# Optimization experiments

Hardware: AMD Instinct MI355X
Metric: run time of the kernel (lower is better)

The kernel has to match this reference:

```python
import jax, jax.numpy as jnp
import numpy as np

N, D, H = 4096, 1024, 16
GAMMA = 1.0


def setup_inputs() -> dict:
    key = jax.random.key(0)
    ks = jax.random.split(key, 10)
    s = 1.0 / np.sqrt(D)
    return {
        "x": jax.random.normal(ks[0], (N, D), jnp.float32),
        "h": jax.random.normal(ks[1], (N,), jnp.float32),
        "Wq": jax.random.normal(ks[2], (D, D), jnp.float32) * s,
        "bq": jax.random.normal(ks[3], (D,), jnp.float32) * s,
        "Wk": jax.random.normal(ks[4], (D, D), jnp.float32) * s,
        "bk": jax.random.normal(ks[5], (D,), jnp.float32) * s,
        "Wv": jax.random.normal(ks[6], (D, D), jnp.float32) * s,
        "bv": jax.random.normal(ks[7], (D,), jnp.float32) * s,
        "Wo": jax.random.normal(ks[8], (D, D), jnp.float32) * s,
        "bo": jax.random.normal(ks[9], (D,), jnp.float32) * s,
    }


def reference(x, h, Wq, bq, Wk, bk, Wv, bv, Wo, bo):
    n, d = x.shape
    d_head = d // H
    # torch Linear: y = x @ W.T + b
    q = (x @ Wq.T + bq).reshape(n, H, d_head)
    k = (x @ Wk.T + bk).reshape(n, H, d_head)
    v = (x @ Wv.T + bv).reshape(n, H, d_head)
    scale = 1.0 / np.sqrt(d_head).astype(np.float32)
    logits = jnp.einsum('nhd,mhd->hnm', q, k) * scale  # (H, n, n)
    logits = logits - (GAMMA * h)[None, None, :]       # per-key additive bias
    attn = jax.nn.softmax(logits, axis=-1)
    out = jnp.einsum('hnm,mhd->nhd', attn, v).reshape(n, d)
    return out @ Wo.T + bo + x
```

## Files before the change

### kernel.cpp

```cpp
#include <hip/hip_runtime.h>
#include <hip/hip_bf16.h>
#include <stdint.h>

#define NTOK 4096
#define DM   1024
#define NH   16
#define DH   64
#define SCL  0.1803368801111129f
#define LOG2E 1.4426950408889634f

typedef __attribute__((ext_vector_type(8)))  short bf16x8;
typedef __attribute__((ext_vector_type(4)))  float f32x4;
typedef __attribute__((ext_vector_type(16))) float f32x16;
typedef __attribute__((ext_vector_type(4)))  unsigned short us4;

__device__ inline unsigned short f2bf(float f) {
  union { float f; unsigned int u; } a;
  a.f = f;
  unsigned int u = a.u;
  u += 0x7fffu + ((u >> 16) & 1u);
  return (unsigned short)(u >> 16);
}

__device__ inline unsigned int cvtpk_bf16(float lo, float hi) {
  unsigned int r;
  asm("v_cvt_pk_bf16_f32 %0, %1, %2" : "=v"(r) : "v"(lo), "v"(hi));
  return r;
}

__device__ inline void gload_lds16(const void* gsrc, void* ldst) {
  __builtin_amdgcn_global_load_lds(
      (const __attribute__((address_space(1))) void*)(uintptr_t)gsrc,
      (__attribute__((address_space(3))) void*)(unsigned int)(uintptr_t)ldst,
      16, 0, 0);
}

__global__ void cvt_kernel(const float* __restrict__ in,
                           unsigned short* __restrict__ out, int n4) {
  int i = blockIdx.x * 256 + threadIdx.x;
  if (i < n4) {
    float4 v = ((const float4*)in)[i];
    us4 o;
    o[0] = f2bf(v.x); o[1] = f2bf(v.y); o[2] = f2bf(v.z); o[3] = f2bf(v.w);
    ((us4*)out)[i] = o;
  }
}

__global__ void hprep_kernel(const float* __restrict__ h,
                             float* __restrict__ hperm) {
  int i = blockIdx.x * 256 + threadIdx.x;
  int r  = i & 15;
  int hi = (i >> 4) & 1;
  int t  = i >> 5;
  int key = t * 32 + (r & 3) + 8 * (r >> 2) + 4 * hi;
  hperm[i] = -LOG2E * h[key];
}

__global__ __launch_bounds__(256)
void gemm_qkv(const unsigned short* __restrict__ A,
              const unsigned short* __restrict__ B,
              const float* __restrict__ bq, const float* __restrict__ bk,
              const float* __restrict__ bv,
              unsigned short* __restrict__ Qb, unsigned short* __restrict__ Kb,
              unsigned short* __restrict__ Vt)
{
  const int tid  = threadIdx.x;
  const int wid  = tid >> 6;
  const int lane = tid & 63;
  const int bn = blockIdx.x * 128;
  const int bm = blockIdx.y * 128;
  const int wr = wid >> 1;
  const int wc = wid & 1;

  __shared__ __align__(16) unsigned short As[128 * 32];
  __shared__ __align__(16) unsigned short Bs[128 * 32];

  f32x4 acc[4][4];
#pragma unroll
  for (int i = 0; i < 4; i++)
#pragma unroll
    for (int j = 0; j < 4; j++) acc[i][j] = f32x4{0.f, 0.f, 0.f, 0.f};

  const int fr = lane & 15;
  const int fk = (lane >> 4) * 8;
  const int srow = lane >> 2;
  const int scol = (lane & 3) * 8;

  for (int k0 = 0; k0 < DM; k0 += 32) {
#pragma unroll
    for (int c = 0; c < 2; ++c) {
      const int chunk = wid * 2 + c;
      gload_lds16(A + (size_t)(bm + chunk * 16 + srow) * DM + k0 + scol,
                  &As[chunk * 512]);
      gload_lds16(B + (size_t)(bn + chunk * 16 + srow) * DM + k0 + scol,
                  &Bs[chunk * 512]);
    }
    __syncthreads();
    bf16x8 af[4], bfr[4];
#pragma unroll
    for (int i = 0; i < 4; i++)
      af[i] = *(const bf16x8*)&As[(wr * 64 + i * 16 + fr) * 32 + fk];
#pragma unroll
    for (int j = 0; j < 4; j++)
      bfr[j] = *(const bf16x8*)&Bs[(wc * 64 + j * 16 + fr) * 32 + fk];
#pragma unroll
    for (int i = 0; i < 4; i++)
#pragma unroll
      for (int j = 0; j < 4; j++)
        acc[i][j] = __builtin_amdgcn_mfma_f32_16x16x32_bf16(af[i], bfr[j],
                                                            acc[i][j], 0, 0, 0);
    __syncthreads();
  }

  const int fq = lane >> 4;
  const int region = bn >> 10;
  const float* bias = (region == 0) ? bq : (region == 1) ? bk : bv;
  const float qscale = (region == 0) ? SCL : 1.0f;
  unsigned short* outp = (region == 0) ? Qb : Kb;
#pragma unroll
  for (int j = 0; j < 4; j++) {
    const int col = bn + wc * 64 + j * 16 + fr;
    const int cl  = col & 1023;
    const float bvx = bias[cl];
#pragma unroll
    for (int i = 0; i < 4; i++) {
      const int row0 = bm + wr * 64 + i * 16 + fq * 4;
      if (region < 2) {
#pragma unroll
        for (int r = 0; r < 4; r++)
          outp[(size_t)(row0 + r) * DM + cl] = f2bf((acc[i][j][r] + bvx) * qscale);
      } else {
        us4 pk;
#pragma unroll
        for (int r = 0; r < 4; r++) pk[r] = f2bf(acc[i][j][r] + bvx);
        *(us4*)&Vt[(size_t)cl * NTOK + row0] = pk;
      }
    }
  }
}

__global__ __launch_bounds__(256)
void gemm_out(const unsigned short* __restrict__ A,
              const unsigned short* __restrict__ B,
              const float* __restrict__ bias,
              const float* __restrict__ resid,
              float* __restrict__ Cf)
{
  const int tid  = threadIdx.x;
  const int wid  = tid >> 6;
  const int lane = tid & 63;
  const int bn = blockIdx.x * 128;
  const int bm = blockIdx.y * 128;
  const int wr = wid >> 1;
  const int wc = wid & 1;

  __shared__ __align__(16) unsigned short As[128 * 32];
  __shared__ __align__(16) unsigned short Bs[128 * 32];

  f32x4 acc[4][4];
#pragma unroll
  for (int i = 0; i < 4; i++)
#pragma unroll
    for (int j = 0; j < 4; j++) acc[i][j] = f32x4{0.f, 0.f, 0.f, 0.f};

  const int fr = lane & 15;
  const int fk = (lane >> 4) * 8;
  const int srow = lane >> 2;
  const int scol = (lane & 3) * 8;

  for (int k0 = 0; k0 < DM; k0 += 32) {
#pragma unroll
    for (int c = 0; c < 2; ++c) {
      const int chunk = wid * 2 + c;
      gload_lds16(A + (size_t)(bm + chunk * 16 + srow) * DM + k0 + scol,
                  &As[chunk * 512]);
      gload_lds16(B + (size_t)(bn + chunk * 16 + srow) * DM + k0 + scol,
                  &Bs[chunk * 512]);
    }
    __syncthreads();
    bf16x8 af[4], bfr[4];
#pragma unroll
    for (int i = 0; i < 4; i++)
      af[i] = *(const bf16x8*)&As[(wr * 64 + i * 16 + fr) * 32 + fk];
#pragma unroll
    for (int j = 0; j < 4; j++)
      bfr[j] = *(const bf16x8*)&Bs[(wc * 64 + j * 16 + fr) * 32 + fk];
#pragma unroll
    for (int i = 0; i < 4; i++)
#pragma unroll
      for (int j = 0; j < 4; j++)
        acc[i][j] = __builtin_amdgcn_mfma_f32_16x16x32_bf16(af[i], bfr[j],
                                                            acc[i][j], 0, 0, 0);
    __syncthreads();
  }

  const int fq = lane >> 4;
#pragma unroll
  for (int j = 0; j < 4; j++) {
    const int col = bn + wc * 64 + j * 16 + fr;
    const float bvx = bias[col];
#pragma unroll
    for (int i = 0; i < 4; i++) {
      const int row0 = bm + wr * 64 + i * 16 + fq * 4;
#pragma unroll
      for (int r = 0; r < 4; r++) {
        const size_t idx = (size_t)(row0 + r) * DM + col;
        Cf[idx] = acc[i][j][r] + bvx + resid[idx];
      }
    }
  }
}

#define MFMA32(a, b, c) __builtin_amdgcn_mfma_f32_32x32x16_bf16(a, b, c, 0, 0, 0)

__global__ void attn_kernel(const unsigned short* __restrict__ Q,
                            const unsigned short* __restrict__ K,
                            const unsigned short* __restrict__ Vt,
                            const float* __restrict__ hperm,
                            unsigned short* __restrict__ O)
{
  const int wgid = (blockIdx.x & 7) * 64 + (blockIdx.x >> 3);
  const int head = wgid >> 5;
  const int tid  = threadIdx.x;
  const int wid  = tid >> 6;
  const int grp  = wid >> 2;
  const int w4   = wid & 3;
  const int lane = tid & 63;
  const int c31  = lane & 31;
  const int hi   = lane >> 5;
  const int qb   = (wgid & 31) * 128 + w4 * 32;
  const int k0g  = grp * (NTOK / 4);

  __shared__ __align__(16) char lds_raw[65536];
  char* kbase = lds_raw + grp * 16384;
  char* vbase = kbase + 8192;

  const int l8 = lane >> 3;
  const int l7 = lane & 7;
  const int sq = l7 ^ l8;
  const unsigned short* kg =
      K + (size_t)(k0g + w4 * 8 + l8) * DM + head * DH + sq * 8;
  const unsigned short* vg =
      Vt + (size_t)(head * DH + (sq >> 2) * 32 + w4 * 8 + l8) * NTOK
         + k0g + (sq & 3) * 8;

  int koffB[4], voffB[2][2];
#pragma unroll
  for (int f = 0; f < 4; f++)
    koffB[f] = c31 * 128 + (((f * 2 + hi) ^ (c31 & 7)) << 4);
#pragma unroll
  for (int db = 0; db < 2; db++)
#pragma unroll
    for (int ko = 0; ko < 2; ko++)
      voffB[db][ko] = c31 * 128 + (((db * 4 + ko * 2 + hi) ^ (c31 & 7)) << 4);

  const unsigned short* qp = Q + (size_t)(qb + c31) * DM + head * DH + hi * 8;
  const bf16x8 qf0 = *(const bf16x8*)(qp);
  const bf16x8 qf1 = *(const bf16x8*)(qp + 16);
  const bf16x8 qf2 = *(const bf16x8*)(qp + 32);
  const bf16x8 qf3 = *(const bf16x8*)(qp + 48);

  f32x16 o0, o1;
#pragma unroll
  for (int i = 0; i < 16; i++) { o0[i] = 0.f; o1[i] = 0.f; }
  float l = 0.f;

  gload_lds16(kg, kbase + w4 * 1024);
  gload_lds16(vg, vbase + w4 * 1024);
  __syncthreads();

  int cur = 0;
  const int NT = NTOK / 4 / 32;
  for (int t = 0; t < NT; ++t) {
    if (t + 1 < NT) {
      gload_lds16(kg + (size_t)(t + 1) * 32 * DM,
                  kbase + (cur ^ 1) * 4096 + w4 * 1024);
      gload_lds16(vg + (t + 1) * 32,
                  vbase + (cur ^ 1) * 4096 + w4 * 1024);
    }

    const float* hp = hperm + k0g + t * 32 + hi * 16;
    const float4 b0 = *(const float4*)(hp + 0);
    const float4 b1 = *(const float4*)(hp + 4);
    const float4 b2 = *(const float4*)(hp + 8);
    const float4 b3 = *(const float4*)(hp + 12);
    f32x16 s;
    s[0]  = b0.x; s[1]  = b0.y; s[2]  = b0.z; s[3]  = b0.w;
    s[4]  = b1.x; s[5]  = b1.y; s[6]  = b1.z; s[7]  = b1.w;
    s[8]  = b2.x; s[9]  = b2.y; s[10] = b2.z; s[11] = b2.w;
    s[12] = b3.x; s[13] = b3.y; s[14] = b3.z; s[15] = b3.w;

    const char* Kb = kbase + cur * 4096;
    const char* Vb = vbase + cur * 4096;
    const bf16x8 kf0 = *(const bf16x8*)(Kb + koffB[0]);
    const bf16x8 kf1 = *(const bf16x8*)(Kb + koffB[1]);
    const bf16x8 kf2 = *(const bf16x8*)(Kb + koffB[2]);
    const bf16x8 kf3 = *(const bf16x8*)(Kb + koffB[3]);
    const bf16x8 v00 = *(const bf16x8*)(Vb + voffB[0][0]);
    const bf16x8 v01 = *(const bf16x8*)(Vb + voffB[0][1]);
    const bf16x8 v10 = *(const bf16x8*)(Vb + voffB[1][0]);
    const bf16x8 v11 = *(const bf16x8*)(Vb + voffB[1][1]);

    s = MFMA32(kf0, qf0, s);
    s = MFMA32(kf1, qf1, s);
    s = MFMA32(kf2, qf2, s);
    s = MFMA32(kf3, qf3, s);

    float ps[16];
#pragma unroll
    for (int r = 0; r < 16; r++) ps[r] = __builtin_amdgcn_exp2f(s[r]);
    const float rs = (((ps[0] + ps[1]) + (ps[2] + ps[3])) +
                      ((ps[4] + ps[5]) + (ps[6] + ps[7]))) +
                     (((ps[8] + ps[9]) + (ps[10] + ps[11])) +
                      ((ps[12] + ps[13]) + (ps[14] + ps[15])));
    l += rs;

    unsigned int X1 = cvtpk_bf16(ps[0],  ps[1]);
    unsigned int X2 = cvtpk_bf16(ps[2],  ps[3]);
    unsigned int Y1 = cvtpk_bf16(ps[4],  ps[5]);
    unsigned int Y2 = cvtpk_bf16(ps[6],  ps[7]);
    asm("v_permlane32_swap_b32 %0, %1" : "+v"(X1), "+v"(Y1));
    asm("v_permlane32_swap_b32 %0, %1" : "+v"(X2), "+v"(Y2));
    unsigned int X3 = cvtpk_bf16(ps[8],  ps[9]);
    unsigned int X4 = cvtpk_bf16(ps[10], ps[11]);
    unsigned int Y3 = cvtpk_bf16(ps[12], ps[13]);
    unsigned int Y4 = cvtpk_bf16(ps[14], ps[15]);
    asm("v_permlane32_swap_b32 %0, %1" : "+v"(X3), "+v"(Y3));
    asm("v_permlane32_swap_b32 %0, %1" : "+v"(X4), "+v"(Y4));

    union { unsigned int u[4]; bf16x8 v; } P0, P1;
    P0.u[0] = X1; P0.u[1] = X2; P0.u[2] = Y1; P0.u[3] = Y2;
    P1.u[0] = X3; P1.u[1] = X4; P1.u[2] = Y3; P1.u[3] = Y4;

    o0 = MFMA32(v00, P0.v, o0);
    o0 = MFMA32(v01, P1.v, o0);
    o1 = MFMA32(v10, P0.v, o1);
    o1 = MFMA32(v11, P1.v, o1);

    __syncthreads();
    cur ^= 1;
  }

  float ov[32];
#pragma unroll
  for (int i = 0; i < 16; i++) { ov[i] = o0[i]; ov[16 + i] = o1[i]; }
  l += __shfl_xor(l, 32, 64);

  float* mO = (float*)lds_raw;
  float* mL = (float*)(lds_raw + 34816);
  const int g2 = grp >> 1;
  float* slotA = &mO[((g2 * 4 + w4) * 64 + lane) * 17];
  const int liA = (g2 * 4 + w4) * 32 + c31;
  float* slotB = &mO[(w4 * 64 + lane) * 17];
  const int liB = w4 * 32 + c31;

#pragma unroll
  for (int H = 0; H < 2; H++) {
    if (grp & 1) {
#pragma unroll
      for (int i = 0; i < 16; i++) slotA[i] = ov[H * 16 + i];
      if (H == 0 && hi == 0) mL[liA] = l;
    }
    __syncthreads();
    if (!(grp & 1)) {
#pragma unroll
      for (int i = 0; i < 16; i++) ov[H * 16 + i] += slotA[i];
      if (H == 0) l += mL[liA];
    }
    __syncthreads();
  }
#pragma unroll
  for (int H = 0; H < 2; H++) {
    if (grp == 2) {
#pragma unroll
      for (int i = 0; i < 16; i++) slotB[i] = ov[H * 16 + i];
      if (H == 0 && hi == 0) mL[liB] = l;
    }
    __syncthreads();
    if (grp == 0) {
#pragma unroll
      for (int i = 0; i < 16; i++) ov[H * 16 + i] += slotB[i];
      if (H == 0) l += mL[liB];
    }
    __syncthreads();
  }

  if (grp == 0) {
    const float inv = 1.0f / l;
    unsigned short* ob = O + (size_t)(qb + c31) * DM + head * DH;
#pragma unroll
    for (int g = 0; g < 4; g++) {
      us4 pk;
      pk[0] = f2bf(ov[4 * g + 0] * inv); pk[1] = f2bf(ov[4 * g + 1] * inv);
      pk[2] = f2bf(ov[4 * g + 2] * inv); pk[3] = f2bf(ov[4 * g + 3] * inv);
      *(us4*)(ob + 8 * g + 4 * hi) = pk;
    }
#pragma unroll
    for (int g = 0; g < 4; g++) {
      us4 pk;
      pk[0] = f2bf(ov[16 + 4 * g + 0] * inv); pk[1] = f2bf(ov[16 + 4 * g + 1] * inv);
      pk[2] = f2bf(ov[16 + 4 * g + 2] * inv); pk[3] = f2bf(ov[16 + 4 * g + 3] * inv);
      *(us4*)(ob + 32 + 8 * g + 4 * hi) = pk;
    }
  }
}

extern "C" void kernel_launch(void* const* d_in, const int* in_sizes, int n_in,
                              void* d_out, int out_size, void* d_ws, size_t ws_size,
                              hipStream_t stream) {
  const float* x  = (const float*)d_in[0];
  const float* h  = (const float*)d_in[1];
  const float* Wq = (const float*)d_in[2];
  const float* bq = (const float*)d_in[3];
  const float* Wk = (const float*)d_in[4];
  const float* bk = (const float*)d_in[5];
  const float* Wv = (const float*)d_in[6];
  const float* bv = (const float*)d_in[7];
  const float* Wo = (const float*)d_in[8];
  const float* bo = (const float*)d_in[9];
  float* out = (float*)d_out;

  char* ws = (char*)d_ws;
  const size_t MB = 1 << 20;
  unsigned short* xb    = (unsigned short*)(ws + 0 * MB);
  unsigned short* wqkvb = (unsigned short*)(ws + 8 * MB);
  unsigned short* wob   = (unsigned short*)(ws + 14 * MB);
  unsigned short* Qb    = (unsigned short*)(ws + 16 * MB);
  unsigned short* Kb    = (unsigned short*)(ws + 24 * MB);
  unsigned short* Vtb   = (unsigned short*)(ws + 32 * MB);
  unsigned short* AOb   = (unsigned short*)(ws + 40 * MB);
  float*          hperm = (float*)(ws + 48 * MB);

  cvt_kernel<<<4096, 256, 0, stream>>>(x,  xb, (NTOK * DM) / 4);
  cvt_kernel<<<1024, 256, 0, stream>>>(Wq, wqkvb,               (DM * DM) / 4);
  cvt_kernel<<<1024, 256, 0, stream>>>(Wk, wqkvb + DM * DM,     (DM * DM) / 4);
  cvt_kernel<<<1024, 256, 0, stream>>>(Wv, wqkvb + 2 * DM * DM, (DM * DM) / 4);
  cvt_kernel<<<1024, 256, 0, stream>>>(Wo, wob,                 (DM * DM) / 4);
  hprep_kernel<<<16, 256, 0, stream>>>(h, hperm);

  gemm_qkv<<<dim3(24, 32), 256, 0, stream>>>(xb, wqkvb, bq, bk, bv, Qb, Kb, Vtb);

  attn_kernel<<<dim3(512), 1024, 0, stream>>>(Qb, Kb, Vtb, hperm, AOb);

  gemm_out<<<dim3(DM / 128, NTOK / 128), 256, 0, stream>>>(AOb, wob, bo, x, out);
}
```

Measured before the change: 188.0 us.

## Double query rows per wave in attention and fuse conversion kernels

The attention kernel now has each wave process two 32-row query tiles, A and B, against every K/V tile loaded into LDS. The block shrinks to 512 threads with two key-split groups, and the grid goes from 512 blocks to 256. Halving the redundant K/V loads and LDS reads per unit of MFMA work should improve reuse and shorten the cross-group reduction, at the cost of more registers and fewer blocks in flight. Separately, the five dtype conversion launches and the h-permutation launch are merged into one fused kernel to cut launch overhead.

```diff
diff --git a/kernel.cpp b/kernel.cpp
--- a/kernel.cpp
+++ b/kernel.cpp
@@ -35,25 +35,37 @@
       16, 0, 0);
 }
 
-__global__ void cvt_kernel(const float* __restrict__ in,
-                           unsigned short* __restrict__ out, int n4) {
-  int i = blockIdx.x * 256 + threadIdx.x;
-  if (i < n4) {
-    float4 v = ((const float4*)in)[i];
-    us4 o;
-    o[0] = f2bf(v.x); o[1] = f2bf(v.y); o[2] = f2bf(v.z); o[3] = f2bf(v.w);
-    ((us4*)out)[i] = o;
-  }
-}
-
-__global__ void hprep_kernel(const float* __restrict__ h,
-                             float* __restrict__ hperm) {
-  int i = blockIdx.x * 256 + threadIdx.x;
-  int r  = i & 15;
-  int hi = (i >> 4) & 1;
-  int t  = i >> 5;
-  int key = t * 32 + (r & 3) + 8 * (r >> 2) + 4 * hi;
-  hperm[i] = -LOG2E * h[key];
+__global__ void cvt_fused(const float* __restrict__ x,
+                          const float* __restrict__ Wq,
+                          const float* __restrict__ Wk,
+                          const float* __restrict__ Wv,
+                          const float* __restrict__ Wo,
+                          const float* __restrict__ h,
+                          unsigned short* __restrict__ xb,
+                          unsigned short* __restrict__ wqkvb,
+                          unsigned short* __restrict__ wob,
+                          float* __restrict__ hperm) {
+  const int b = blockIdx.x;
+  if (b >= 8192) {
+    int i = (b - 8192) * 256 + threadIdx.x;
+    int r  = i & 15;
+    int hh = (i >> 4) & 1;
+    int t  = i >> 5;
+    int key = t * 32 + (r & 3) + 8 * (r >> 2) + 4 * hh;
+    hperm[i] = -LOG2E * h[key];
+    return;
+  }
+  int i = b * 256 + threadIdx.x;
+  const float* src; unsigned short* dst; int off;
+  if (i < 1048576)      { src = x;  dst = xb;                 off = i; }
+  else if (i < 1310720) { src = Wq; dst = wqkvb;              off = i - 1048576; }
+  else if (i < 1572864) { src = Wk; dst = wqkvb + DM * DM;    off = i - 1310720; }
+  else if (i < 1835008) { src = Wv; dst = wqkvb + 2 * DM * DM; off = i - 1572864; }
+  else                  { src = Wo; dst = wob;                off = i - 1835008; }
+  float4 v = ((const float4*)src)[off];
+  us4 o;
+  o[0] = f2bf(v.x); o[1] = f2bf(v.y); o[2] = f2bf(v.z); o[3] = f2bf(v.w);
+  ((us4*)dst)[off] = o;
 }
 
 __global__ __launch_bounds__(256)
@@ -213,14 +225,16 @@
 
 #define MFMA32(a, b, c) __builtin_amdgcn_mfma_f32_32x32x16_bf16(a, b, c, 0, 0, 0)
 
-__global__ void attn_kernel(const unsigned short* __restrict__ Q,
-                            const unsigned short* __restrict__ K,
-                            const unsigned short* __restrict__ Vt,
-                            const float* __restrict__ hperm,
-                            unsigned short* __restrict__ O)
+__global__ __launch_bounds__(512)
+void attn_kernel(const unsigned short* __restrict__ Q,
+                 const unsigned short* __restrict__ K,
+                 const unsigned short* __restrict__ Vt,
+                 const float* __restrict__ hperm,
+                 unsigned short* __restrict__ O)
 {
-  const int wgid = (blockIdx.x & 7) * 64 + (blockIdx.x >> 3);
-  const int head = wgid >> 5;
+  const int wgid = (blockIdx.x & 7) * 32 + (blockIdx.x >> 3);
+  const int head = wgid >> 4;
+  const int qblk = wgid & 15;
   const int tid  = threadIdx.x;
   const int wid  = tid >> 6;
   const int grp  = wid >> 2;
@@ -228,49 +242,58 @@
   const int lane = tid & 63;
   const int c31  = lane & 31;
   const int hi   = lane >> 5;
-  const int qb   = (wgid & 31) * 128 + w4 * 32;
-  const int k0g  = grp * (NTOK / 4);
-
-  __shared__ __align__(16) char lds_raw[65536];
+  const int qwb  = qblk * 256 + w4 * 64;
+  const int k0g  = grp * 2048;
+
+  __shared__ __align__(16) char lds_raw[34816];
   char* kbase = lds_raw + grp * 16384;
   char* vbase = kbase + 8192;
 
-  const int l8 = lane >> 3;
-  const int l7 = lane & 7;
-  const int sq = l7 ^ l8;
+  const int srow = w4 * 4 + (lane >> 4);
+  const int ssl  = lane & 15;
+  const int kq   = ssl ^ srow;
+  const int kkey = srow + 16 * (kq >> 3);
   const unsigned short* kg =
-      K + (size_t)(k0g + w4 * 8 + l8) * DM + head * DH + sq * 8;
+      K + (size_t)(k0g + kkey) * DM + head * DH + (kq & 7) * 8;
+  const int vd = ((kq) >> 2) * 16 + srow;
   const unsigned short* vg =
-      Vt + (size_t)(head * DH + (sq >> 2) * 32 + w4 * 8 + l8) * NTOK
-         + k0g + (sq & 3) * 8;
-
+      Vt + (size_t)(head * DH + vd) * NTOK + k0g + (kq & 3) * 8;
+
+  const int fr15 = c31 & 15;
+  const int fkh  = c31 >> 4;
   int koffB[4], voffB[2][2];
 #pragma unroll
   for (int f = 0; f < 4; f++)
-    koffB[f] = c31 * 128 + (((f * 2 + hi) ^ (c31 & 7)) << 4);
+    koffB[f] = fr15 * 256 + (((fkh * 8 + f * 2 + hi) ^ fr15) << 4);
 #pragma unroll
   for (int db = 0; db < 2; db++)
 #pragma unroll
     for (int ko = 0; ko < 2; ko++)
-      voffB[db][ko] = c31 * 128 + (((db * 4 + ko * 2 + hi) ^ (c31 & 7)) << 4);
-
-  const unsigned short* qp = Q + (size_t)(qb + c31) * DM + head * DH + hi * 8;
-  const bf16x8 qf0 = *(const bf16x8*)(qp);
-  const bf16x8 qf1 = *(const bf16x8*)(qp + 16);
-  const bf16x8 qf2 = *(const bf16x8*)(qp + 32);
-  const bf16x8 qf3 = *(const bf16x8*)(qp + 48);
-
-  f32x16 o0, o1;
-#pragma unroll
-  for (int i = 0; i < 16; i++) { o0[i] = 0.f; o1[i] = 0.f; }
-  float l = 0.f;
+      voffB[db][ko] =
+          fr15 * 256 + ((((db * 2 + fkh) * 4 + ko * 2 + hi) ^ fr15) << 4);
+
+  const unsigned short* qpA = Q + (size_t)(qwb + c31) * DM + head * DH + hi * 8;
+  const unsigned short* qpB = qpA + (size_t)32 * DM;
+  const bf16x8 qa0 = *(const bf16x8*)(qpA);
+  const bf16x8 qa1 = *(const bf16x8*)(qpA + 16);
+  const bf16x8 qa2 = *(const bf16x8*)(qpA + 32);
+  const bf16x8 qa3 = *(const bf16x8*)(qpA + 48);
+  const bf16x8 qb0 = *(const bf16x8*)(qpB);
+  const bf16x8 qb1 = *(const bf16x8*)(qpB + 16);
+  const bf16x8 qb2 = *(const bf16x8*)(qpB + 32);
+  const bf16x8 qb3 = *(const bf16x8*)(qpB + 48);
+
+  f32x16 o0A, o1A, o0B, o1B;
+#pragma unroll
+  for (int i = 0; i < 16; i++) { o0A[i] = 0.f; o1A[i] = 0.f; o0B[i] = 0.f; o1B[i] = 0.f; }
+  float lA = 0.f, lB = 0.f;
 
   gload_lds16(kg, kbase + w4 * 1024);
   gload_lds16(vg, vbase + w4 * 1024);
   __syncthreads();
 
   int cur = 0;
-  const int NT = NTOK / 4 / 32;
+  const int NT = 2048 / 32;
   for (int t = 0; t < NT; ++t) {
     if (t + 1 < NT) {
       gload_lds16(kg + (size_t)(t + 1) * 32 * DM,
@@ -284,11 +307,6 @@
     const float4 b1 = *(const float4*)(hp + 4);
     const float4 b2 = *(const float4*)(hp + 8);
     const float4 b3 = *(const float4*)(hp + 12);
-    f32x16 s;
-    s[0]  = b0.x; s[1]  = b0.y; s[2]  = b0.z; s[3]  = b0.w;
-    s[4]  = b1.x; s[5]  = b1.y; s[6]  = b1.z; s[7]  = b1.w;
-    s[8]  = b2.x; s[9]  = b2.y; s[10] = b2.z; s[11] = b2.w;
-    s[12] = b3.x; s[13] = b3.y; s[14] = b3.z; s[15] = b3.w;
 
     const char* Kb = kbase + cur * 4096;
     const char* Vb = vbase + cur * 4096;
@@ -296,25 +314,35 @@
     const bf16x8 kf1 = *(const bf16x8*)(Kb + koffB[1]);
     const bf16x8 kf2 = *(const bf16x8*)(Kb + koffB[2]);
     const bf16x8 kf3 = *(const bf16x8*)(Kb + koffB[3]);
+
+    f32x16 sA, sB;
+    sA[0]  = b0.x; sA[1]  = b0.y; sA[2]  = b0.z; sA[3]  = b0.w;
+    sA[4]  = b1.x; sA[5]  = b1.y; sA[6]  = b1.z; sA[7]  = b1.w;
+    sA[8]  = b2.x; sA[9]  = b2.y; sA[10] = b2.z; sA[11] = b2.w;
+    sA[12] = b3.x; sA[13] = b3.y; sA[14] = b3.z; sA[15] = b3.w;
+    sB = sA;
+
+    sA = MFMA32(kf0, qa0, sA);
+    sA = MFMA32(kf1, qa1, sA);
+    sA = MFMA32(kf2, qa2, sA);
+    sA = MFMA32(kf3, qa3, sA);
+    sB = MFMA32(kf0, qb0, sB);
+    sB = MFMA32(kf1, qb1, sB);
+    sB = MFMA32(kf2, qb2, sB);
+    sB = MFMA32(kf3, qb3, sB);
+
     const bf16x8 v00 = *(const bf16x8*)(Vb + voffB[0][0]);
     const bf16x8 v01 = *(const bf16x8*)(Vb + voffB[0][1]);
     const bf16x8 v10 = *(const bf16x8*)(Vb + voffB[1][0]);
     const bf16x8 v11 = *(const bf16x8*)(Vb + voffB[1][1]);
 
-    s = MFMA32(kf0, qf0, s);
-    s = MFMA32(kf1, qf1, s);
-    s = MFMA32(kf2, qf2, s);
-    s = MFMA32(kf3, qf3, s);
-
     float ps[16];
 #pragma unroll
-    for (int r = 0; r < 16; r++) ps[r] = __builtin_amdgcn_exp2f(s[r]);
-    const float rs = (((ps[0] + ps[1]) + (ps[2] + ps[3])) +
-                      ((ps[4] + ps[5]) + (ps[6] + ps[7]))) +
-                     (((ps[8] + ps[9]) + (ps[10] + ps[11])) +
-                      ((ps[12] + ps[13]) + (ps[14] + ps[15])));
-    l += rs;
-
+    for (int r = 0; r < 16; r++) ps[r] = __builtin_amdgcn_exp2f(sA[r]);
+    lA += (((ps[0] + ps[1]) + (ps[2] + ps[3])) +
+           ((ps[4] + ps[5]) + (ps[6] + ps[7]))) +
+          (((ps[8] + ps[9]) + (ps[10] + ps[11])) +
+           ((ps[12] + ps[13]) + (ps[14] + ps[15])));
     unsigned int X1 = cvtpk_bf16(ps[0],  ps[1]);
     unsigned int X2 = cvtpk_bf16(ps[2],  ps[3]);
     unsigned int Y1 = cvtpk_bf16(ps[4],  ps[5]);
@@ -327,80 +355,97 @@
     unsigned int Y4 = cvtpk_bf16(ps[14], ps[15]);
     asm("v_permlane32_swap_b32 %0, %1" : "+v"(X3), "+v"(Y3));
     asm("v_permlane32_swap_b32 %0, %1" : "+v"(X4), "+v"(Y4));
-
-    union { unsigned int u[4]; bf16x8 v; } P0, P1;
-    P0.u[0] = X1; P0.u[1] = X2; P0.u[2] = Y1; P0.u[3] = Y2;
-    P1.u[0] = X3; P1.u[1] = X4; P1.u[2] = Y3; P1.u[3] = Y4;
-
-    o0 = MFMA32(v00, P0.v, o0);
-    o0 = MFMA32(v01, P1.v, o0);
-    o1 = MFMA32(v10, P0.v, o1);
-    o1 = MFMA32(v11, P1.v, o1);
+    union { unsigned int u[4]; bf16x8 v; } PA0, PA1;
+    PA0.u[0] = X1; PA0.u[1] = X2; PA0.u[2] = Y1; PA0.u[3] = Y2;
+    PA1.u[0] = X3; PA1.u[1] = X4; PA1.u[2] = Y3; PA1.u[3] = Y4;
+
+#pragma unroll
+    for (int r = 0; r < 16; r++) ps[r] = __builtin_amdgcn_exp2f(sB[r]);
+    lB += (((ps[0] + ps[1]) + (ps[2] + ps[3])) +
+           ((ps[4] + ps[5]) + (ps[6] + ps[7]))) +
+          (((ps[8] + ps[9]) + (ps[10] + ps[11])) +
+           ((ps[12] + ps[13]) + (ps[14] + ps[15])));
+    X1 = cvtpk_bf16(ps[0],  ps[1]);
+    X2 = cvtpk_bf16(ps[2],  ps[3]);
+    Y1 = cvtpk_bf16(ps[4],  ps[5]);
+    Y2 = cvtpk_bf16(ps[6],  ps[7]);
+    asm("v_permlane32_swap_b32 %0, %1" : "+v"(X1), "+v"(Y1));
+    asm("v_permlane32_swap_b32 %0, %1" : "+v"(X2), "+v"(Y2));
+    X3 = cvtpk_bf16(ps[8],  ps[9]);
+    X4 = cvtpk_bf16(ps[10], ps[11]);
+    Y3 = cvtpk_bf16(ps[12], ps[13]);
+    Y4 = cvtpk_bf16(ps[14], ps[15]);
+    asm("v_permlane32_swap_b32 %0, %1" : "+v"(X3), "+v"(Y3));
+    asm("v_permlane32_swap_b32 %0, %1" : "+v"(X4), "+v"(Y4));
+    union { unsigned int u[4]; bf16x8 v; } PB0, PB1;
+    PB0.u[0] = X1; PB0.u[1] = X2; PB0.u[2] = Y1; PB0.u[3] = Y2;
+    PB1.u[0] = X3; PB1.u[1] = X4; PB1.u[2] = Y3; PB1.u[3] = Y4;
+
+    o0A = MFMA32(v00, PA0.v, o0A);
+    o0A = MFMA32(v01, PA1.v, o0A);
+    o1A = MFMA32(v10, PA0.v, o1A);
+    o1A = MFMA32(v11, PA1.v, o1A);
+    o0B = MFMA32(v00, PB0.v, o0B);
+    o0B = MFMA32(v01, PB1.v, o0B);
+    o1B = MFMA32(v10, PB0.v, o1B);
+    o1B = MFMA32(v11, PB1.v, o1B);
 
     __syncthreads();
     cur ^= 1;
   }
 
-  float ov[32];
-#pragma unroll
-  for (int i = 0; i < 16; i++) { ov[i] = o0[i]; ov[16 + i] = o1[i]; }
-  l += __shfl_xor(l, 32, 64);
-
-  float* mO = (float*)lds_raw;
-  float* mL = (float*)(lds_raw + 34816);
-  const int g2 = grp >> 1;
-  float* slotA = &mO[((g2 * 4 + w4) * 64 + lane) * 17];
-  const int liA = (g2 * 4 + w4) * 32 + c31;
-  float* slotB = &mO[(w4 * 64 + lane) * 17];
-  const int liB = w4 * 32 + c31;
-
-#pragma unroll
-  for (int H = 0; H < 2; H++) {
-    if (grp & 1) {
-#pragma unroll
-      for (int i = 0; i < 16; i++) slotA[i] = ov[H * 16 + i];
-      if (H == 0 && hi == 0) mL[liA] = l;
-    }
-    __syncthreads();
-    if (!(grp & 1)) {
-#pragma unroll
-      for (int i = 0; i < 16; i++) ov[H * 16 + i] += slotA[i];
-      if (H == 0) l += mL[liA];
-    }
-    __syncthreads();
-  }
-#pragma unroll
-  for (int H = 0; H < 2; H++) {
-    if (grp == 2) {
-#pragma unroll
-      for (int i = 0; i < 16; i++) slotB[i] = ov[H * 16 + i];
-      if (H == 0 && hi == 0) mL[liB] = l;
+  lA += __shfl_xor(lA, 32, 64);
+  lB += __shfl_xor(lB, 32, 64);
+
+  float* mo = (float*)lds_raw;
+  float* mL = (float*)(lds_raw + 33792);
+  float* row = &mo[(w4 * 64 + lane) * 33];
+#pragma unroll
+  for (int half = 0; half < 2; half++) {
+    __syncthreads();
+    if (grp == 1) {
+      const f32x16& hA = half ? o1A : o0A;
+      const f32x16& hB = half ? o1B : o0B;
+#pragma unroll
+      for (int i = 0; i < 16; i++) { row[i] = hA[i]; row[16 + i] = hB[i]; }
+      if (half == 0 && hi == 0) {
+        mL[(w4 * 2 + 0) * 32 + c31] = lA;
+        mL[(w4 * 2 + 1) * 32 + c31] = lB;
+      }
     }
     __syncthreads();
     if (grp == 0) {
-#pragma unroll
-      for (int i = 0; i < 16; i++) ov[H * 16 + i] += slotB[i];
-      if (H == 0) l += mL[liB];
-    }
-    __syncthreads();
+      f32x16& hA = half ? o1A : o0A;
+      f32x16& hB = half ? o1B : o0B;
+#pragma unroll
+      for (int i = 0; i < 16; i++) { hA[i] += row[i]; hB[i] += row[16 + i]; }
+      if (half == 0) {
+        lA += mL[(w4 * 2 + 0) * 32 + c31];
+        lB += mL[(w4 * 2 + 1) * 32 + c31];
+      }
+    }
   }
 
   if (grp == 0) {
-    const float inv = 1.0f / l;
-    unsigned short* ob = O + (size_t)(qb + c31) * DM + head * DH;
+    const float invA = 1.0f / lA;
+    const float invB = 1.0f / lB;
+    unsigned short* obA = O + (size_t)(qwb + c31) * DM + head * DH;
+    unsigned short* obB = obA + (size_t)32 * DM;
 #pragma unroll
     for (int g = 0; g < 4; g++) {
       us4 pk;
-      pk[0] = f2bf(ov[4 * g + 0] * inv); pk[1] = f2bf(ov[4 * g + 1] * inv);
-      pk[2] = f2bf(ov[4 * g + 2] * inv); pk[3] = f2bf(ov[4 * g + 3] * inv);
-      *(us4*)(ob + 8 * g + 4 * hi) = pk;
-    }
-#pragma unroll
-    for (int g = 0; g < 4; g++) {
-      us4 pk;
-      pk[0] = f2bf(ov[16 + 4 * g + 0] * inv); pk[1] = f2bf(ov[16 + 4 * g + 1] * inv);
-      pk[2] = f2bf(ov[16 + 4 * g + 2] * inv); pk[3] = f2bf(ov[16 + 4 * g + 3] * inv);
-      *(us4*)(ob + 32 + 8 * g + 4 * hi) = pk;
+      pk[0] = f2bf(o0A[4 * g + 0] * invA); pk[1] = f2bf(o0A[4 * g + 1] * invA);
+      pk[2] = f2bf(o0A[4 * g + 2] * invA); pk[3] = f2bf(o0A[4 * g + 3] * invA);
+      *(us4*)(obA + 8 * g + 4 * hi) = pk;
+      pk[0] = f2bf(o1A[4 * g + 0] * invA); pk[1] = f2bf(o1A[4 * g + 1] * invA);
+      pk[2] = f2bf(o1A[4 * g + 2] * invA); pk[3] = f2bf(o1A[4 * g + 3] * invA);
+      *(us4*)(obA + 32 + 8 * g + 4 * hi) = pk;
+      pk[0] = f2bf(o0B[4 * g + 0] * invB); pk[1] = f2bf(o0B[4 * g + 1] * invB);
+      pk[2] = f2bf(o0B[4 * g + 2] * invB); pk[3] = f2bf(o0B[4 * g + 3] * invB);
+      *(us4*)(obB + 8 * g + 4 * hi) = pk;
+      pk[0] = f2bf(o1B[4 * g + 0] * invB); pk[1] = f2bf(o1B[4 * g + 1] * invB);
+      pk[2] = f2bf(o1B[4 * g + 2] * invB); pk[3] = f2bf(o1B[4 * g + 3] * invB);
+      *(us4*)(obB + 32 + 8 * g + 4 * hi) = pk;
     }
   }
 }
@@ -431,16 +476,12 @@
   unsigned short* AOb   = (unsigned short*)(ws + 40 * MB);
   float*          hperm = (float*)(ws + 48 * MB);
 
-  cvt_kernel<<<4096, 256, 0, stream>>>(x,  xb, (NTOK * DM) / 4);
-  cvt_kernel<<<1024, 256, 0, stream>>>(Wq, wqkvb,               (DM * DM) / 4);
-  cvt_kernel<<<1024, 256, 0, stream>>>(Wk, wqkvb + DM * DM,     (DM * DM) / 4);
-  cvt_kernel<<<1024, 256, 0, stream>>>(Wv, wqkvb + 2 * DM * DM, (DM * DM) / 4);
-  cvt_kernel<<<1024, 256, 0, stream>>>(Wo, wob,                 (DM * DM) / 4);
-  hprep_kernel<<<16, 256, 0, stream>>>(h, hperm);
+  cvt_fused<<<8208, 256, 0, stream>>>(x, Wq, Wk, Wv, Wo, h,
+                                      xb, wqkvb, wob, hperm);
 
   gemm_qkv<<<dim3(24, 32), 256, 0, stream>>>(xb, wqkvb, bq, bk, bv, Qb, Kb, Vtb);
 
-  attn_kernel<<<dim3(512), 1024, 0, stream>>>(Qb, Kb, Vtb, hperm, AOb);
+  attn_kernel<<<dim3(256), 512, 0, stream>>>(Qb, Kb, Vtb, hperm, AOb);
 
   gemm_out<<<dim3(DM / 128, NTOK / 128), 256, 0, stream>>>(AOb, wob, bo, x, out);
 }
```

Measured after the change: 169.2 us. 1.11x faster.

## Halve attention workgroup to two key groups and fuse conversion kernels

Applied to the files above, without the earlier changes.

The attention kernel drops from 1024 to 512 threads per workgroup, so two key-split groups of 2048 keys each run instead of four groups of 1024. LDS shrinks to 32KB, the K/V staging layout and swizzle change to a 16-row pattern, and the cross-group reduction becomes a single step. The five fp32-to-bf16 conversion launches and the h-prep launch are merged into one kernel to cut launch overhead. Each workgroup now runs longer serial loops with fewer waves, but smaller LDS and launch bounds could allow more workgroups per CU.

```diff
diff --git a/kernel.cpp b/kernel.cpp
--- a/kernel.cpp
+++ b/kernel.cpp
@@ -35,25 +35,37 @@
       16, 0, 0);
 }
 
-__global__ void cvt_kernel(const float* __restrict__ in,
-                           unsigned short* __restrict__ out, int n4) {
-  int i = blockIdx.x * 256 + threadIdx.x;
-  if (i < n4) {
-    float4 v = ((const float4*)in)[i];
-    us4 o;
-    o[0] = f2bf(v.x); o[1] = f2bf(v.y); o[2] = f2bf(v.z); o[3] = f2bf(v.w);
-    ((us4*)out)[i] = o;
-  }
-}
-
-__global__ void hprep_kernel(const float* __restrict__ h,
-                             float* __restrict__ hperm) {
-  int i = blockIdx.x * 256 + threadIdx.x;
-  int r  = i & 15;
-  int hi = (i >> 4) & 1;
-  int t  = i >> 5;
-  int key = t * 32 + (r & 3) + 8 * (r >> 2) + 4 * hi;
-  hperm[i] = -LOG2E * h[key];
+__global__ void cvt_fused(const float* __restrict__ x,
+                          const float* __restrict__ Wq,
+                          const float* __restrict__ Wk,
+                          const float* __restrict__ Wv,
+                          const float* __restrict__ Wo,
+                          const float* __restrict__ h,
+                          unsigned short* __restrict__ xb,
+                          unsigned short* __restrict__ wqkvb,
+                          unsigned short* __restrict__ wob,
+                          float* __restrict__ hperm) {
+  const int b = blockIdx.x;
+  if (b >= 8192) {
+    int i = (b - 8192) * 256 + threadIdx.x;
+    int r  = i & 15;
+    int hh = (i >> 4) & 1;
+    int t  = i >> 5;
+    int key = t * 32 + (r & 3) + 8 * (r >> 2) + 4 * hh;
+    hperm[i] = -LOG2E * h[key];
+    return;
+  }
+  int i = b * 256 + threadIdx.x;
+  const float* src; unsigned short* dst; int off;
+  if (i < 1048576)      { src = x;  dst = xb;                 off = i; }
+  else if (i < 1310720) { src = Wq; dst = wqkvb;              off = i - 1048576; }
+  else if (i < 1572864) { src = Wk; dst = wqkvb + DM * DM;    off = i - 1310720; }
+  else if (i < 1835008) { src = Wv; dst = wqkvb + 2 * DM * DM; off = i - 1572864; }
+  else                  { src = Wo; dst = wob;                off = i - 1835008; }
+  float4 v = ((const float4*)src)[off];
+  us4 o;
+  o[0] = f2bf(v.x); o[1] = f2bf(v.y); o[2] = f2bf(v.z); o[3] = f2bf(v.w);
+  ((us4*)dst)[off] = o;
 }
 
 __global__ __launch_bounds__(256)
@@ -213,14 +225,16 @@
 
 #define MFMA32(a, b, c) __builtin_amdgcn_mfma_f32_32x32x16_bf16(a, b, c, 0, 0, 0)
 
-__global__ void attn_kernel(const unsigned short* __restrict__ Q,
-                            const unsigned short* __restrict__ K,
-                            const unsigned short* __restrict__ Vt,
-                            const float* __restrict__ hperm,
-                            unsigned short* __restrict__ O)
+__global__ __launch_bounds__(512)
+void attn_kernel(const unsigned short* __restrict__ Q,
+                 const unsigned short* __restrict__ K,
+                 const unsigned short* __restrict__ Vt,
+                 const float* __restrict__ hperm,
+                 unsigned short* __restrict__ O)
 {
   const int wgid = (blockIdx.x & 7) * 64 + (blockIdx.x >> 3);
   const int head = wgid >> 5;
+  const int qblk = wgid & 31;
   const int tid  = threadIdx.x;
   const int wid  = tid >> 6;
   const int grp  = wid >> 2;
@@ -228,33 +242,37 @@
   const int lane = tid & 63;
   const int c31  = lane & 31;
   const int hi   = lane >> 5;
-  const int qb   = (wgid & 31) * 128 + w4 * 32;
-  const int k0g  = grp * (NTOK / 4);
-
-  __shared__ __align__(16) char lds_raw[65536];
+  const int qwb  = qblk * 128 + w4 * 32;
+  const int k0g  = grp * 2048;
+
+  __shared__ __align__(16) char lds_raw[32768];
   char* kbase = lds_raw + grp * 16384;
   char* vbase = kbase + 8192;
 
-  const int l8 = lane >> 3;
-  const int l7 = lane & 7;
-  const int sq = l7 ^ l8;
+  const int srow = w4 * 4 + (lane >> 4);
+  const int ssl  = lane & 15;
+  const int kq   = ssl ^ srow;
+  const int kkey = srow + 16 * (kq >> 3);
   const unsigned short* kg =
-      K + (size_t)(k0g + w4 * 8 + l8) * DM + head * DH + sq * 8;
+      K + (size_t)(k0g + kkey) * DM + head * DH + (kq & 7) * 8;
+  const int vd = (kq >> 2) * 16 + srow;
   const unsigned short* vg =
-      Vt + (size_t)(head * DH + (sq >> 2) * 32 + w4 * 8 + l8) * NTOK
-         + k0g + (sq & 3) * 8;
-
+      Vt + (size_t)(head * DH + vd) * NTOK + k0g + (kq & 3) * 8;
+
+  const int fr15 = c31 & 15;
+  const int fkh  = c31 >> 4;
   int koffB[4], voffB[2][2];
 #pragma unroll
   for (int f = 0; f < 4; f++)
-    koffB[f] = c31 * 128 + (((f * 2 + hi) ^ (c31 & 7)) << 4);
+    koffB[f] = fr15 * 256 + (((fkh * 8 + f * 2 + hi) ^ fr15) << 4);
 #pragma unroll
   for (int db = 0; db < 2; db++)
 #pragma unroll
     for (int ko = 0; ko < 2; ko++)
-      voffB[db][ko] = c31 * 128 + (((db * 4 + ko * 2 + hi) ^ (c31 & 7)) << 4);
-
-  const unsigned short* qp = Q + (size_t)(qb + c31) * DM + head * DH + hi * 8;
+      voffB[db][ko] =
+          fr15 * 256 + ((((db * 2 + fkh) * 4 + ko * 2 + hi) ^ fr15) << 4);
+
+  const unsigned short* qp = Q + (size_t)(qwb + c31) * DM + head * DH + hi * 8;
   const bf16x8 qf0 = *(const bf16x8*)(qp);
   const bf16x8 qf1 = *(const bf16x8*)(qp + 16);
   const bf16x8 qf2 = *(const bf16x8*)(qp + 32);
@@ -270,7 +288,7 @@
   __syncthreads();
 
   int cur = 0;
-  const int NT = NTOK / 4 / 32;
+  const int NT = 2048 / 32;
   for (int t = 0; t < NT; ++t) {
     if (t + 1 < NT) {
       gload_lds16(kg + (size_t)(t + 1) * 32 * DM,
@@ -284,11 +302,6 @@
     const float4 b1 = *(const float4*)(hp + 4);
     const float4 b2 = *(const float4*)(hp + 8);
     const float4 b3 = *(const float4*)(hp + 12);
-    f32x16 s;
-    s[0]  = b0.x; s[1]  = b0.y; s[2]  = b0.z; s[3]  = b0.w;
-    s[4]  = b1.x; s[5]  = b1.y; s[6]  = b1.z; s[7]  = b1.w;
-    s[8]  = b2.x; s[9]  = b2.y; s[10] = b2.z; s[11] = b2.w;
-    s[12] = b3.x; s[13] = b3.y; s[14] = b3.z; s[15] = b3.w;
 
     const char* Kb = kbase + cur * 4096;
     const char* Vb = vbase + cur * 4096;
@@ -296,24 +309,30 @@
     const bf16x8 kf1 = *(const bf16x8*)(Kb + koffB[1]);
     const bf16x8 kf2 = *(const bf16x8*)(Kb + koffB[2]);
     const bf16x8 kf3 = *(const bf16x8*)(Kb + koffB[3]);
+
+    f32x16 s;
+    s[0]  = b0.x; s[1]  = b0.y; s[2]  = b0.z; s[3]  = b0.w;
+    s[4]  = b1.x; s[5]  = b1.y; s[6]  = b1.z; s[7]  = b1.w;
+    s[8]  = b2.x; s[9]  = b2.y; s[10] = b2.z; s[11] = b2.w;
+    s[12] = b3.x; s[13] = b3.y; s[14] = b3.z; s[15] = b3.w;
+
+    s = MFMA32(kf0, qf0, s);
+    s = MFMA32(kf1, qf1, s);
+    s = MFMA32(kf2, qf2, s);
+    s = MFMA32(kf3, qf3, s);
+
     const bf16x8 v00 = *(const bf16x8*)(Vb + voffB[0][0]);
     const bf16x8 v01 = *(const bf16x8*)(Vb + voffB[0][1]);
     const bf16x8 v10 = *(const bf16x8*)(Vb + voffB[1][0]);
     const bf16x8 v11 = *(const bf16x8*)(Vb + voffB[1][1]);
 
-    s = MFMA32(kf0, qf0, s);
-    s = MFMA32(kf1, qf1, s);
-    s = MFMA32(kf2, qf2, s);
-    s = MFMA32(kf3, qf3, s);
-
     float ps[16];
 #pragma unroll
     for (int r = 0; r < 16; r++) ps[r] = __builtin_amdgcn_exp2f(s[r]);
-    const float rs = (((ps[0] + ps[1]) + (ps[2] + ps[3])) +
-                      ((ps[4] + ps[5]) + (ps[6] + ps[7]))) +
-                     (((ps[8] + ps[9]) + (ps[10] + ps[11])) +
-                      ((ps[12] + ps[13]) + (ps[14] + ps[15])));
-    l += rs;
+    l += (((ps[0] + ps[1]) + (ps[2] + ps[3])) +
+          ((ps[4] + ps[5]) + (ps[6] + ps[7]))) +
+         (((ps[8] + ps[9]) + (ps[10] + ps[11])) +
+          ((ps[12] + ps[13]) + (ps[14] + ps[15])));
 
     unsigned int X1 = cvtpk_bf16(ps[0],  ps[1]);
     unsigned int X2 = cvtpk_bf16(ps[2],  ps[3]);
@@ -341,65 +360,40 @@
     cur ^= 1;
   }
 
-  float ov[32];
-#pragma unroll
-  for (int i = 0; i < 16; i++) { ov[i] = o0[i]; ov[16 + i] = o1[i]; }
   l += __shfl_xor(l, 32, 64);
 
-  float* mO = (float*)lds_raw;
-  float* mL = (float*)(lds_raw + 34816);
-  const int g2 = grp >> 1;
-  float* slotA = &mO[((g2 * 4 + w4) * 64 + lane) * 17];
-  const int liA = (g2 * 4 + w4) * 32 + c31;
-  float* slotB = &mO[(w4 * 64 + lane) * 17];
-  const int liB = w4 * 32 + c31;
-
-#pragma unroll
-  for (int H = 0; H < 2; H++) {
-    if (grp & 1) {
-#pragma unroll
-      for (int i = 0; i < 16; i++) slotA[i] = ov[H * 16 + i];
-      if (H == 0 && hi == 0) mL[liA] = l;
-    }
-    __syncthreads();
-    if (!(grp & 1)) {
-#pragma unroll
-      for (int i = 0; i < 16; i++) ov[H * 16 + i] += slotA[i];
-      if (H == 0) l += mL[liA];
-    }
-    __syncthreads();
-  }
-#pragma unroll
-  for (int H = 0; H < 2; H++) {
-    if (grp == 2) {
-#pragma unroll
-      for (int i = 0; i < 16; i++) slotB[i] = ov[H * 16 + i];
-      if (H == 0 && hi == 0) mL[liB] = l;
+  float* mo = (float*)lds_raw;
+  float* mL = (float*)(lds_raw + 17408);
+  float* row = &mo[(w4 * 64 + lane) * 17];
+#pragma unroll
+  for (int half = 0; half < 2; half++) {
+    __syncthreads();
+    if (grp == 1) {
+      const f32x16& hA = half ? o1 : o0;
+#pragma unroll
+      for (int i = 0; i < 16; i++) row[i] = hA[i];
+      if (half == 0 && hi == 0) mL[w4 * 32 + c31] = l;
     }
     __syncthreads();
     if (grp == 0) {
-#pragma unroll
-      for (int i = 0; i < 16; i++) ov[H * 16 + i] += slotB[i];
-      if (H == 0) l += mL[liB];
-    }
-    __syncthreads();
+      f32x16& hA = half ? o1 : o0;
+#pragma unroll
+      for (int i = 0; i < 16; i++) hA[i] += row[i];
+      if (half == 0) l += mL[w4 * 32 + c31];
+    }
   }
 
   if (grp == 0) {
     const float inv = 1.0f / l;
-    unsigned short* ob = O + (size_t)(qb + c31) * DM + head * DH;
+    unsigned short* ob = O + (size_t)(qwb + c31) * DM + head * DH;
 #pragma unroll
     for (int g = 0; g < 4; g++) {
       us4 pk;
-      pk[0] = f2bf(ov[4 * g + 0] * inv); pk[1] = f2bf(ov[4 * g + 1] * inv);
-      pk[2] = f2bf(ov[4 * g + 2] * inv); pk[3] = f2bf(ov[4 * g + 3] * inv);
+      pk[0] = f2bf(o0[4 * g + 0] * inv); pk[1] = f2bf(o0[4 * g + 1] * inv);
+      pk[2] = f2bf(o0[4 * g + 2] * inv); pk[3] = f2bf(o0[4 * g + 3] * inv);
       *(us4*)(ob + 8 * g + 4 * hi) = pk;
-    }
-#pragma unroll
-    for (int g = 0; g < 4; g++) {
-      us4 pk;
-      pk[0] = f2bf(ov[16 + 4 * g + 0] * inv); pk[1] = f2bf(ov[16 + 4 * g + 1] * inv);
-      pk[2] = f2bf(ov[16 + 4 * g + 2] * inv); pk[3] = f2bf(ov[16 + 4 * g + 3] * inv);
+      pk[0] = f2bf(o1[4 * g + 0] * inv); pk[1] = f2bf(o1[4 * g + 1] * inv);
+      pk[2] = f2bf(o1[4 * g + 2] * inv); pk[3] = f2bf(o1[4 * g + 3] * inv);
       *(us4*)(ob + 32 + 8 * g + 4 * hi) = pk;
     }
   }
@@ -431,16 +425,12 @@
   unsigned short* AOb   = (unsigned short*)(ws + 40 * MB);
   float*          hperm = (float*)(ws + 48 * MB);
 
-  cvt_kernel<<<4096, 256, 0, stream>>>(x,  xb, (NTOK * DM) / 4);
-  cvt_kernel<<<1024, 256, 0, stream>>>(Wq, wqkvb,               (DM * DM) / 4);
-  cvt_kernel<<<1024, 256, 0, stream>>>(Wk, wqkvb + DM * DM,     (DM * DM) / 4);
-  cvt_kernel<<<1024, 256, 0, stream>>>(Wv, wqkvb + 2 * DM * DM, (DM * DM) / 4);
-  cvt_kernel<<<1024, 256, 0, stream>>>(Wo, wob,                 (DM * DM) / 4);
-  hprep_kernel<<<16, 256, 0, stream>>>(h, hperm);
+  cvt_fused<<<8208, 256, 0, stream>>>(x, Wq, Wk, Wv, Wo, h,
+                                      xb, wqkvb, wob, hperm);
 
   gemm_qkv<<<dim3(24, 32), 256, 0, stream>>>(xb, wqkvb, bq, bk, bv, Qb, Kb, Vtb);
 
-  attn_kernel<<<dim3(512), 1024, 0, stream>>>(Qb, Kb, Vtb, hperm, AOb);
+  attn_kernel<<<dim3(512), 512, 0, stream>>>(Qb, Kb, Vtb, hperm, AOb);
 
   gemm_out<<<dim3(DM / 128, NTOK / 128), 256, 0, stream>>>(AOb, wob, bo, x, out);
 }
```

Measured after the change: 169.6 us. 1.11x faster.
